# Kernel optimization log

Measured on AMD Instinct MI355X. Metric: run time of the kernel, lower is better.

The kernel has to match this reference:

```python
import jax, jax.numpy as jnp
import numpy as np

B, N_BOX, NUM_CLASSES = 32, 50, 20
FEATURE_SIZES = np.array([[52, 52], [26, 26], [13, 13]])
NUM_CENG = FEATURE_SIZES[:, 0] * FEATURE_SIZES[:, 1]            # [2704, 676, 169]
NUM_TOTAL = int((NUM_CENG * 3).sum())                            # 10647
ANCS_SCALE = np.array([[10, 13], [16, 30], [33, 23], [30, 61], [62, 45],
                       [59, 119], [116, 90], [156, 198], [373, 326]], dtype=np.float32) / 416.0
NEG_IOU_THRESHOLD = 0.5
NUM_NEG = 1000
EPS = 1e-7

def _build_anchor_grid():
    # rows ordered: level(52,26,13) -> cell (row-major) -> 3 anchors per cell
    out = []
    for lvl in range(3):
        f = int(FEATURE_SIZES[lvl, 0])
        ys, xs = np.meshgrid(np.arange(f), np.arange(f), indexing='ij')
        xy = (np.stack([xs, ys], -1).reshape(-1, 2).astype(np.float32)) / f  # cell corner (col/f,row/f)
        xy3 = np.repeat(xy, 3, axis=0)                                       # [f*f*3, 2]
        wh3 = np.tile(ANCS_SCALE[lvl * 3:(lvl + 1) * 3], (f * f, 1))
        out.append(np.concatenate([xy3, wh3], 1))
    return np.concatenate(out, 0)                                            # [10647, 4]

ANCS = jnp.asarray(_build_anchor_grid())
FSIZES = jnp.asarray(np.repeat(FEATURE_SIZES[:, 0].astype(np.float32), NUM_CENG * 3))  # [10647]
OFF_CENG = jnp.asarray([0.0, 2704.0, 3380.0])   # prefix sums of NUM_CENG
FW_LVL = jnp.asarray([52.0, 26.0, 13.0])


def _xywh2ltrb(xywh):
    return jnp.concatenate([xywh[..., :2] - xywh[..., 2:] * 0.5,
                            xywh[..., :2] + xywh[..., 2:] * 0.5], -1)


def _ciou(a, b):
    # a, b: broadcastable [..., 4] ltrb -> CIoU [...]
    lt = jnp.maximum(a[..., :2], b[..., :2])
    rb = jnp.minimum(a[..., 2:], b[..., 2:])
    wh = jnp.clip(rb - lt, 0.0)
    inter = wh[..., 0] * wh[..., 1]
    wa = a[..., 2] - a[..., 0]; ha = a[..., 3] - a[..., 1]
    wb = b[..., 2] - b[..., 0]; hb = b[..., 3] - b[..., 1]
    union = wa * ha + wb * hb - inter
    iou = inter / (union + EPS)
    clt = jnp.minimum(a[..., :2], b[..., :2])
    crb = jnp.maximum(a[..., 2:], b[..., 2:])
    cwh = crb - clt
    c2 = cwh[..., 0] ** 2 + cwh[..., 1] ** 2 + EPS
    ctr_a = (a[..., :2] + a[..., 2:]) * 0.5
    ctr_b = (b[..., :2] + b[..., 2:]) * 0.5
    rho2 = jnp.sum((ctr_a - ctr_b) ** 2, -1)
    v = (4.0 / (jnp.pi ** 2)) * (jnp.arctan(wa / (ha + EPS)) - jnp.arctan(wb / (hb + EPS))) ** 2
    alpha = jax.lax.stop_gradient(v / (1.0 - iou + v + EPS))
    return iou - rho2 / c2 - alpha * v


def _bce(p, t):
    p = jnp.clip(p, EPS, 1.0 - EPS)
    return -(t * jnp.log(p) + (1.0 - t) * jnp.log(1.0 - p))


def _per_image(p, boxes, labels):
    # p: [10647, 25], boxes: [N,4] ltrb, labels: [N] (1-based)
    N = boxes.shape[0]
    bxy = (boxes[:, :2] + boxes[:, 2:]) * 0.5
    bwh = boxes[:, 2:] - boxes[:, :2]
    # ---- anchor-target matching (source's loop always takes argmax anchor) ----
    p1xy = jnp.repeat(bxy, 9, axis=0)                                       # [N*9, 2]
    fpairs = jnp.repeat(jnp.asarray(FEATURE_SIZES, jnp.float32), 3, axis=0)  # [9, 2]
    p2f = jnp.tile(fpairs, (N, 1))                                          # [N*9, 2]
    colrow = jnp.floor(p1xy * p2f)                                          # (col, row) per box/anchor
    anc_xy = colrow / p2f
    anc_wh = jnp.tile(jnp.asarray(ANCS_SCALE), (N, 1))
    anc_ltrb = _xywh2ltrb(jnp.concatenate([anc_xy, anc_wh], 1))
    ids = jnp.arange(N, dtype=boxes.dtype)
    iou_m = _ciou(boxes[:, None, :] + ids[:, None, None],
                  anc_ltrb[None, :, :] + jnp.repeat(ids, 9)[None, :, None])  # [N, N*9]
    k = jnp.argmax(iou_m, axis=1) % 9                                       # best anchor id 0..8
    lvl = k // 3                                                            # (source quirk: //len(NUMS_ANC))
    cr = colrow[jnp.arange(N) * 9 + k]                                      # [N, 2]
    off_cr = cr[:, 1] * FW_LVL[lvl] + cr[:, 0]
    midx = ((OFF_CENG[lvl] + off_cr) * 3.0 + lvl.astype(jnp.float32)).astype(jnp.int32)  # [N]
    # ---- decode predictions ----
    p_box_xy = p[:, :2] / FSIZES[:, None] + ANCS[:, :2]
    p_box_wh = jnp.exp(p[:, 2:4]) * ANCS[:, 2:]
    p_ltrb = _xywh2ltrb(jnp.concatenate([p_box_xy, p_box_wh], -1))          # [10647, 4]
    # ---- positive losses ----
    pcls = p[midx, 5:]                                                      # [N, C]
    t = jax.nn.one_hot(labels - 1, NUM_CLASSES, dtype=pcls.dtype)
    l_cls = _bce(pcls, t).sum()
    pconf = p[midx, 4]
    l_conf_p = (-jnp.log(jnp.clip(pconf, EPS, 1.0 - EPS))).sum()
    ciou_pos = _ciou(boxes, p_ltrb[midx])                                   # [N]
    w = 2.0 - bwh[:, 0] * bwh[:, 1]
    l_box = (w * (1.0 - ciou_pos)).sum()
    # ---- negative conf loss (replicates filtered-coordinate indexing) ----
    iou_all = _ciou(boxes[:, None, :], p_ltrb[None, :, :])                  # [N, 10647]
    mx = iou_all.max(axis=0)
    mask = mx < NEG_IOU_THRESHOLD
    key = jnp.where(mask, mx, jnp.inf)
    order = jnp.argsort(key)                                                # masked-in first, ascending
    rank = jnp.cumsum(mask) - 1                                             # filtered coordinate per row
    neg_idx = rank[order][:NUM_NEG]                                         # == source's _max_index[:NUM_NEG]
    pneg = p[neg_idx, 4]
    l_conf_n = (-jnp.log(jnp.clip(1.0 - pneg, EPS, 1.0 - EPS))).sum()
    nf = jnp.asarray(N, p.dtype)
    return l_cls / nf, l_box / nf, l_conf_p / nf, l_conf_n


def setup_inputs() -> dict:
    key = jax.random.key(0)
    k1, k2, k3, k4 = jax.random.split(key, 4)
    p_yolo_ts = jax.random.uniform(k1, (B, NUM_TOTAL, 4 + 1 + NUM_CLASSES),
                                   dtype=jnp.float32, minval=1e-4, maxval=1.0 - 1e-4)
    cxy = jax.random.uniform(k2, (B, N_BOX, 2), minval=0.15, maxval=0.85)
    wh = jax.random.uniform(k3, (B, N_BOX, 2), minval=0.05, maxval=0.25)
    boxes = jnp.concatenate([cxy - wh * 0.5, cxy + wh * 0.5], -1).astype(jnp.float32)
    labels = jax.random.randint(k4, (B, N_BOX), 1, NUM_CLASSES + 1, dtype=jnp.int32)
    return {"p_yolo_ts": p_yolo_ts, "boxes": boxes, "labels": labels}


def reference(p_yolo_ts, boxes, labels):
    l_cls, l_box, l_cp, l_cn = jax.vmap(_per_image)(p_yolo_ts, boxes, labels)
    return l_cp.mean() + l_cn.mean() + l_box.mean() + l_cls.mean()
```

## Files before the change

### kernel.cpp

```cpp
#include <hip/hip_runtime.h>

namespace {

constexpr int BB   = 32;
constexpr int NBOX = 50;
constexpr int NCLS = 20;
constexpr int NT   = 10647;
constexpr int NNEG = 1000;
constexpr int DEC_BLOCKS = (NT + 63) / 64;
constexpr int POS_BLOCKS = (NBOX + 3) / 4;
constexpr float EPS = 1e-7f;
constexpr float PI4 = (float)(4.0 / 9.869604401089358);

__device__ __constant__ float c_aw[9] = {10.f/416.f,16.f/416.f,33.f/416.f,30.f/416.f,62.f/416.f,59.f/416.f,116.f/416.f,156.f/416.f,373.f/416.f};
__device__ __constant__ float c_ah[9] = {13.f/416.f,30.f/416.f,23.f/416.f,61.f/416.f,45.f/416.f,119.f/416.f,90.f/416.f,198.f/416.f,326.f/416.f};

__device__ __forceinline__ float fastrcp(float x) {
  return __builtin_amdgcn_rcpf(x);
}

__device__ __forceinline__ float dciou(float al, float at, float ar, float ab,
                                       float bl, float bt, float br, float bb,
                                       float atanA, float atanB) {
  float ltx = fmaxf(al, bl), lty = fmaxf(at, bt);
  float rbx = fminf(ar, br), rby = fminf(ab, bb);
  float wx = fmaxf(rbx - ltx, 0.f), wy = fmaxf(rby - lty, 0.f);
  float inter = wx * wy;
  float wa = ar - al, ha = ab - at;
  float wb = br - bl, hb = bb - bt;
  float uni = wa * ha + wb * hb - inter;
  float iou = inter / (uni + EPS);
  float cw = fmaxf(ar, br) - fminf(al, bl);
  float ch = fmaxf(ab, bb) - fminf(at, bt);
  float c2 = cw * cw + ch * ch + EPS;
  float dx = (al + ar) * 0.5f - (bl + br) * 0.5f;
  float dy = (at + ab) * 0.5f - (bt + bb) * 0.5f;
  float rho2 = dx * dx + dy * dy;
  float dat = atanA - atanB;
  float v = PI4 * (dat * dat);
  float alpha = v / (1.f - iou + v + EPS);
  return iou - rho2 / c2 - alpha * v;
}

__device__ __forceinline__ float dciou_h(float4 A, float4 E,
                                         float bl, float bt, float br, float bb,
                                         float areaB,
                                         float cxb, float cyb, float atanB) {
  float ltx = fmaxf(A.x, bl), lty = fmaxf(A.y, bt);
  float rbx = fminf(A.z, br), rby = fminf(A.w, bb);
  float wx = fmaxf(rbx - ltx, 0.f), wy = fmaxf(rby - lty, 0.f);
  float inter = wx * wy;
  float uni = E.w + areaB - inter;
  float iou = inter * fastrcp(uni + EPS);
  float cw = fmaxf(A.z, br) - fminf(A.x, bl);
  float ch = fmaxf(A.w, bb) - fminf(A.y, bt);
  float c2 = cw * cw + ch * ch + EPS;
  float dx = E.x - cxb;
  float dy = E.y - cyb;
  float rho2 = dx * dx + dy * dy;
  float dat = E.z - atanB;
  float v = PI4 * (dat * dat);
  float alpha = v * fastrcp(1.f - iou + v + EPS);
  return iou - rho2 * fastrcp(c2) - alpha * v;
}

__device__ __forceinline__ int wave_incl_scan(int x, int lane) {
  #pragma unroll
  for (int off = 1; off < 64; off <<= 1) {
    int y = __shfl_up(x, off);
    if (lane >= off) x += y;
  }
  return x;
}

__global__ __launch_bounds__(256) void k_main(const float* __restrict__ p,
                            const float* __restrict__ boxes,
                            const int* __restrict__ labels,
                            unsigned long long* __restrict__ comp,
                            float* __restrict__ pcls, float* __restrict__ pbox,
                            float* __restrict__ pcp) {
  const int b = blockIdx.y;
  const int tid = threadIdx.x;

  if (blockIdx.x < DEC_BLOCKS) {
    __shared__ float4 sA[NBOX];
    __shared__ float4 sE[NBOX];
    if (tid < NBOX) {
      const float* bp = boxes + (b * NBOX + tid) * 4;
      float l = bp[0], t = bp[1], r = bp[2], d = bp[3];
      sA[tid] = make_float4(l, t, r, d);
      float wa = r - l, ha = d - t;
      sE[tid] = make_float4((l + r) * 0.5f, (t + d) * 0.5f,
                            atanf(wa / (ha + EPS)), wa * ha);
    }
    __syncthreads();

    const int q = tid & 3;
    const int j = blockIdx.x * 64 + (tid >> 2);
    if (j >= NT) return;

    int lvl = (j < 8112) ? 0 : ((j < 10140) ? 1 : 2);
    int jb0 = (lvl == 0) ? 0 : ((lvl == 1) ? 8112 : 10140);
    int f   = (lvl == 0) ? 52 : ((lvl == 1) ? 26 : 13);
    int jj = j - jb0;
    int cell = jj / 3, a = jj % 3 + lvl * 3;
    int x = cell % f, y = cell / f;
    float ff = (float)f;
    const float* pr = p + ((size_t)b * NT + j) * 25;
    float px = pr[0] / ff + (float)x / ff;
    float py = pr[1] / ff + (float)y / ff;
    float pw = expf(pr[2]) * c_aw[a];
    float ph = expf(pr[3]) * c_ah[a];
    float bl = px - pw * 0.5f, bt = py - ph * 0.5f;
    float br = px + pw * 0.5f, bbv = py + ph * 0.5f;
    float wb = br - bl, hb = bbv - bt;
    float areab = wb * hb;
    float cxb = (bl + br) * 0.5f, cyb = (bt + bbv) * 0.5f;
    float atb = atanf(wb / (hb + EPS));

    float mx = -INFINITY;
    #pragma unroll 4
    for (int i = q; i < NBOX; i += 4) {
      float v = dciou_h(sA[i], sE[i], bl, bt, br, bbv, areab, cxb, cyb, atb);
      mx = fmaxf(mx, v);
    }
    mx = fmaxf(mx, __shfl_xor(mx, 1));
    mx = fmaxf(mx, __shfl_xor(mx, 2));

    if (q == 0) {
      float key = (mx < 0.5f) ? mx : INFINITY;
      unsigned int u = __float_as_uint(key);
      u = (u & 0x80000000u) ? ~u : (u | 0x80000000u);
      comp[(size_t)b * NT + j] = ((unsigned long long)u << 14) | (unsigned long long)j;
    }
  } else {
    const int lane = tid & 63;
    const int wave = tid >> 6;
    const int i = (blockIdx.x - DEC_BLOCKS) * 4 + wave;

    __shared__ float scx[NBOX], scy[NBOX];
    if (tid < NBOX) {
      const float* bp = boxes + (b * NBOX + tid) * 4;
      float l = bp[0], t = bp[1], r = bp[2], d = bp[3];
      scx[tid] = (l + r) * 0.5f;
      scy[tid] = (t + d) * 0.5f;
    }
    __syncthreads();
    if (i >= NBOX) return;

    const float* bi = boxes + (b * NBOX + i) * 4;
    float bl0 = bi[0], bt0 = bi[1], br0 = bi[2], bd0 = bi[3];
    float fi = (float)i;
    float al = bl0 + fi, at = bt0 + fi, ar = br0 + fi, ad = bd0 + fi;
    float wa = ar - al, ha = ad - at;
    float atanA = atanf(wa / (ha + EPS));

    float bestv = -INFINITY; int bestm = 1 << 30;
    #pragma unroll
    for (int m = lane; m < 9 * NBOX; m += 64) {
      int jb = m / 9, aa = m % 9;
      float fa = (aa < 3) ? 52.f : (aa < 6 ? 26.f : 13.f);
      float col = floorf(scx[jb] * fa);
      float row = floorf(scy[jb] * fa);
      float ax = col / fa, ay = row / fa;
      float aw = c_aw[aa], ah = c_ah[aa];
      float fj = (float)jb;
      float bl = (ax - aw * 0.5f) + fj;
      float bt = (ay - ah * 0.5f) + fj;
      float br = (ax + aw * 0.5f) + fj;
      float bd = (ay + ah * 0.5f) + fj;
      float wb = br - bl, hb = bd - bt;
      float atanB = atanf(wb / (hb + EPS));
      float v = dciou(al, at, ar, ad, bl, bt, br, bd, atanA, atanB);
      if (v > bestv) { bestv = v; bestm = m; }
    }
    #pragma unroll
    for (int off = 32; off > 0; off >>= 1) {
      float ov = __shfl_down(bestv, off);
      int om = __shfl_down(bestm, off);
      if (ov > bestv || (ov == bestv && om < bestm)) { bestv = ov; bestm = om; }
    }
    int bm = __shfl(bestm, 0);

    int k = bm % 9;
    int lvl = k / 3;
    float fk = (k < 3) ? 52.f : (k < 6 ? 26.f : 13.f);
    float col = floorf(scx[i] * fk);
    float row = floorf(scy[i] * fk);
    float offc = (lvl == 0) ? 0.f : (lvl == 1 ? 2704.f : 3380.f);
    int midx = (int)((offc + row * fk + col) * 3.0f + (float)lvl);

    const float* prm = p + ((size_t)b * NT + midx) * 25;
    int lab = labels[b * NBOX + i] - 1;

    float lc = 0.f;
    if (lane < NCLS) {
      float pc = prm[5 + lane];
      pc = fminf(fmaxf(pc, EPS), 1.f - EPS);
      float tt = (lane == lab) ? 1.f : 0.f;
      lc = -(tt * logf(pc) + (1.f - tt) * logf(1.f - pc));
    }
    #pragma unroll
    for (int off = 32; off > 0; off >>= 1) lc += __shfl_down(lc, off);

    if (lane == 0) {
      pcls[b * NBOX + i] = lc;
      float pc4 = prm[4];
      pc4 = fminf(fmaxf(pc4, EPS), 1.f - EPS);
      pcp[b * NBOX + i] = -logf(pc4);

      int lvl2 = (midx < 8112) ? 0 : ((midx < 10140) ? 1 : 2);
      int jb0 = (lvl2 == 0) ? 0 : ((lvl2 == 1) ? 8112 : 10140);
      int f2  = (lvl2 == 0) ? 52 : ((lvl2 == 1) ? 26 : 13);
      int jj2 = midx - jb0;
      int cell2 = jj2 / 3, a2 = jj2 % 3 + lvl2 * 3;
      int xx = cell2 % f2, yy = cell2 / f2;
      float ff2 = (float)f2;
      float px = prm[0] / ff2 + (float)xx / ff2;
      float py = prm[1] / ff2 + (float)yy / ff2;
      float pw = expf(prm[2]) * c_aw[a2];
      float ph = expf(prm[3]) * c_ah[a2];
      float pbl = px - pw * 0.5f, pbt = py - ph * 0.5f;
      float pbr = px + pw * 0.5f, pbd = py + ph * 0.5f;

      float wb = pbr - pbl, hb = pbd - pbt;
      float atanB = atanf(wb / (hb + EPS));
      float wa0 = br0 - bl0, ha0 = bd0 - bt0;
      float atanA0 = atanf(wa0 / (ha0 + EPS));
      float cp = dciou(bl0, bt0, br0, bd0, pbl, pbt, pbr, pbd, atanA0, atanB);
      float w = 2.f - wa0 * ha0;
      pbox[b * NBOX + i] = w * (1.f - cp);
    }
  }
}

__global__ __launch_bounds__(1024) void k_neg2(const unsigned long long* __restrict__ comp,
                                               const float* __restrict__ p,
                                               float* __restrict__ lcn) {
  int b = blockIdx.x;
  const unsigned long long* c = comp + (size_t)b * NT;
  const int tid = threadIdx.x, lane = tid & 63, wave = tid >> 6;

  __shared__ int hist[4096];
  __shared__ int s_w[16];
  __shared__ unsigned long long s_pref;
  __shared__ int s_rem;
  __shared__ int s_digit;
  __shared__ int s_rem_next;
  __shared__ int s_cnt;
  __shared__ float s_facc[16];
  __shared__ int s_tot[11][16];
  __shared__ int s_off[11][16];

  unsigned long long v[11];
  #pragma unroll
  for (int k = 0; k < 11; ++k) {
    int j = k * 1024 + tid;
    v[k] = (j < NT) ? c[j] : ~0ull;
  }

  int wincl[11];
  #pragma unroll
  for (int k = 0; k < 11; ++k) {
    unsigned long long x = v[k];
    int flag = ((x >> 14) < 0xFF800000ull) ? 1 : 0;
    int incl = wave_incl_scan(flag, lane);
    wincl[k] = incl;
    if (lane == 63) s_tot[k][wave] = incl;
  }
  __syncthreads();
  if (wave == 0) {
    int i0 = lane * 3;
    int a0 = (i0     < 176) ? s_tot[i0 / 16][i0 % 16] : 0;
    int a1 = (i0 + 1 < 176) ? s_tot[(i0 + 1) / 16][(i0 + 1) % 16] : 0;
    int a2 = (i0 + 2 < 176) ? s_tot[(i0 + 2) / 16][(i0 + 2) % 16] : 0;
    int lsum = a0 + a1 + a2;
    int linc = wave_incl_scan(lsum, lane);
    int lexc = linc - lsum;
    if (i0     < 176) s_off[i0 / 16][i0 % 16] = lexc;
    if (i0 + 1 < 176) s_off[(i0 + 1) / 16][(i0 + 1) % 16] = lexc + a0;
    if (i0 + 2 < 176) s_off[(i0 + 2) / 16][(i0 + 2) % 16] = lexc + a0 + a1;
    if (lane == 63) s_cnt = linc;
  }
  if (tid == 0) { s_pref = 0ull; s_rem = NNEG - 1; }
  __syncthreads();
  const bool spec = (s_cnt >= NNEG);

  for (int pass = 0; pass < 4; ++pass) {
    int lo = 36 - pass * 12;
    for (int h = tid; h < 4096; h += 1024) hist[h] = 0;
    __syncthreads();
    unsigned long long pref = s_pref;
    #pragma unroll
    for (int k = 0; k < 11; ++k) {
      unsigned long long x = v[k];
      bool fin = ((x >> 14) < 0xFF800000ull);
      if ((!spec || fin) && (x >> (lo + 12)) == (pref >> (lo + 12)))
        atomicAdd(&hist[(int)((x >> lo) & 4095ull)], 1);
    }
    __syncthreads();
    int base = tid * 4;
    int c0 = hist[base], c1 = hist[base + 1], c2 = hist[base + 2], c3 = hist[base + 3];
    int tsum = c0 + c1 + c2 + c3;
    int incl = wave_incl_scan(tsum, lane);
    if (lane == 63) s_w[wave] = incl;
    __syncthreads();
    if (wave == 0) {
      int wv = (lane < 16) ? s_w[lane] : 0;
      int wincl2 = wave_incl_scan(wv, lane);
      if (lane < 16) s_w[lane] = wincl2 - wv;
    }
    __syncthreads();
    int excl = incl - tsum + s_w[wave];
    int rem = s_rem;
    int p0 = excl, p1 = p0 + c0, p2 = p1 + c1, p3 = p2 + c2;
    if (rem >= p0 && rem < p0 + c0) { s_digit = base + 0; s_rem_next = rem - p0; }
    if (rem >= p1 && rem < p1 + c1) { s_digit = base + 1; s_rem_next = rem - p1; }
    if (rem >= p2 && rem < p2 + c2) { s_digit = base + 2; s_rem_next = rem - p2; }
    if (rem >= p3 && rem < p3 + c3) { s_digit = base + 3; s_rem_next = rem - p3; }
    __syncthreads();
    if (tid == 0) {
      s_pref |= ((unsigned long long)s_digit) << lo;
      s_rem = s_rem_next;
    }
    __syncthreads();
  }
  const unsigned long long T = s_pref;

  float acc = 0.f;
  const float* pb = p + (size_t)b * NT * 25;
  #pragma unroll
  for (int k = 0; k < 11; ++k) {
    unsigned long long x = v[k];
    if (x <= T) {
      int idx = s_off[k][wave] + wincl[k] - 1;
      if (idx < 0) idx += NT;
      float q = 1.f - pb[(size_t)idx * 25 + 4];
      q = fminf(fmaxf(q, EPS), 1.f - EPS);
      acc += -logf(q);
    }
  }

  #pragma unroll
  for (int off = 32; off > 0; off >>= 1) acc += __shfl_down(acc, off);
  if (lane == 0) s_facc[wave] = acc;
  __syncthreads();
  if (tid == 0) {
    float s = 0.f;
    #pragma unroll
    for (int w = 0; w < 16; ++w) s += s_facc[w];
    lcn[b] = s;
  }
}

__global__ void k_final(const float* __restrict__ pcls, const float* __restrict__ pbox,
                        const float* __restrict__ pcp, const float* __restrict__ lcn,
                        float* __restrict__ out) {
  int lane = threadIdx.x;
  float s = 0.f;
  if (lane < BB) {
    float a = 0.f, bx = 0.f, cp = 0.f;
    for (int i = 0; i < NBOX; ++i) {
      a  += pcls[lane * NBOX + i];
      bx += pbox[lane * NBOX + i];
      cp += pcp[lane * NBOX + i];
    }
    s = (a + bx + cp) / (float)NBOX + lcn[lane];
  }
  #pragma unroll
  for (int off = 32; off > 0; off >>= 1) s += __shfl_down(s, off);
  if (lane == 0) out[0] = s / (float)BB;
}

}

extern "C" void kernel_launch(void* const* d_in, const int* in_sizes, int n_in,
                              void* d_out, int out_size, void* d_ws, size_t ws_size,
                              hipStream_t stream) {
  const float* p      = (const float*)d_in[0];
  const float* boxes  = (const float*)d_in[1];
  const int*   labels = (const int*)d_in[2];
  float* out = (float*)d_out;

  char* ws = (char*)d_ws;
  size_t off = 0;
  unsigned long long* comp = (unsigned long long*)(ws + off); off += (size_t)BB * NT * sizeof(unsigned long long);
  float* pcls = (float*)(ws + off);                off += BB * NBOX * sizeof(float);
  float* pbox = (float*)(ws + off);                off += BB * NBOX * sizeof(float);
  float* pcp  = (float*)(ws + off);                off += BB * NBOX * sizeof(float);
  float* lcn  = (float*)(ws + off);                off += BB * sizeof(float);

  dim3 g1(DEC_BLOCKS + POS_BLOCKS, BB);
  k_main<<<g1, 256, 0, stream>>>(p, boxes, labels, comp, pcls, pbox, pcp);
  k_neg2<<<BB, 1024, 0, stream>>>(comp, p, lcn);
  k_final<<<1, 64, 0, stream>>>(pcls, pbox, pcp, lcn, out);
}
```

Before: 63.01 us.

## Fuse final reduction into negative-loss kernel and halve threads per anchor

```diff
diff --git a/kernel.cpp b/kernel.cpp
--- a/kernel.cpp
+++ b/kernel.cpp
@@ -7,7 +7,7 @@
 constexpr int NCLS = 20;
 constexpr int NT   = 10647;
 constexpr int NNEG = 1000;
-constexpr int DEC_BLOCKS = (NT + 63) / 64;
+constexpr int DEC_BLOCKS = (NT + 127) / 128;
 constexpr int POS_BLOCKS = (NBOX + 3) / 4;
 constexpr float EPS = 1e-7f;
 constexpr float PI4 = (float)(4.0 / 9.869604401089358);
@@ -78,9 +78,10 @@
                             const int* __restrict__ labels,
                             unsigned long long* __restrict__ comp,
                             float* __restrict__ pcls, float* __restrict__ pbox,
-                            float* __restrict__ pcp) {
+                            float* __restrict__ pcp, float* __restrict__ out) {
   const int b = blockIdx.y;
   const int tid = threadIdx.x;
+  if (blockIdx.x == 0 && b == 0 && tid == 0) out[0] = 0.f;
 
   if (blockIdx.x < DEC_BLOCKS) {
     __shared__ float4 sA[NBOX];
@@ -95,8 +96,8 @@
     }
     __syncthreads();
 
-    const int q = tid & 3;
-    const int j = blockIdx.x * 64 + (tid >> 2);
+    const int par = tid & 1;
+    const int j = blockIdx.x * 128 + (tid >> 1);
     if (j >= NT) return;
 
     int lvl = (j < 8112) ? 0 : ((j < 10140) ? 1 : 2);
@@ -119,15 +120,14 @@
     float atb = atanf(wb / (hb + EPS));
 
     float mx = -INFINITY;
-    #pragma unroll 4
-    for (int i = q; i < NBOX; i += 4) {
+    #pragma unroll 5
+    for (int i = par; i < NBOX; i += 2) {
       float v = dciou_h(sA[i], sE[i], bl, bt, br, bbv, areab, cxb, cyb, atb);
       mx = fmaxf(mx, v);
     }
     mx = fmaxf(mx, __shfl_xor(mx, 1));
-    mx = fmaxf(mx, __shfl_xor(mx, 2));
-
-    if (q == 0) {
+
+    if (par == 0) {
       float key = (mx < 0.5f) ? mx : INFINITY;
       unsigned int u = __float_as_uint(key);
       u = (u & 0x80000000u) ? ~u : (u | 0x80000000u);
@@ -236,7 +236,10 @@
 
 __global__ __launch_bounds__(1024) void k_neg2(const unsigned long long* __restrict__ comp,
                                                const float* __restrict__ p,
-                                               float* __restrict__ lcn) {
+                                               const float* __restrict__ pcls,
+                                               const float* __restrict__ pbox,
+                                               const float* __restrict__ pcp,
+                                               float* __restrict__ out) {
   int b = blockIdx.x;
   const unsigned long long* c = comp + (size_t)b * NT;
   const int tid = threadIdx.x, lane = tid & 63, wave = tid >> 6;
@@ -249,6 +252,7 @@
   __shared__ int s_rem_next;
   __shared__ int s_cnt;
   __shared__ float s_facc[16];
+  __shared__ float s_lcn;
   __shared__ int s_tot[11][16];
   __shared__ int s_off[11][16];
 
@@ -349,27 +353,19 @@
     float s = 0.f;
     #pragma unroll
     for (int w = 0; w < 16; ++w) s += s_facc[w];
-    lcn[b] = s;
-  }
-}
-
-__global__ void k_final(const float* __restrict__ pcls, const float* __restrict__ pbox,
-                        const float* __restrict__ pcp, const float* __restrict__ lcn,
-                        float* __restrict__ out) {
-  int lane = threadIdx.x;
-  float s = 0.f;
-  if (lane < BB) {
-    float a = 0.f, bx = 0.f, cp = 0.f;
-    for (int i = 0; i < NBOX; ++i) {
-      a  += pcls[lane * NBOX + i];
-      bx += pbox[lane * NBOX + i];
-      cp += pcp[lane * NBOX + i];
-    }
-    s = (a + bx + cp) / (float)NBOX + lcn[lane];
-  }
-  #pragma unroll
-  for (int off = 32; off > 0; off >>= 1) s += __shfl_down(s, off);
-  if (lane == 0) out[0] = s / (float)BB;
+    s_lcn = s;
+  }
+  __syncthreads();
+
+  if (wave == 0) {
+    float s3 = 0.f;
+    if (lane < NBOX)
+      s3 = pcls[b * NBOX + lane] + pbox[b * NBOX + lane] + pcp[b * NBOX + lane];
+    #pragma unroll
+    for (int off = 32; off > 0; off >>= 1) s3 += __shfl_down(s3, off);
+    if (lane == 0)
+      atomicAdd(out, (s3 / (float)NBOX + s_lcn) / (float)BB);
+  }
 }
 
 }
@@ -388,10 +384,8 @@
   float* pcls = (float*)(ws + off);                off += BB * NBOX * sizeof(float);
   float* pbox = (float*)(ws + off);                off += BB * NBOX * sizeof(float);
   float* pcp  = (float*)(ws + off);                off += BB * NBOX * sizeof(float);
-  float* lcn  = (float*)(ws + off);                off += BB * sizeof(float);
 
   dim3 g1(DEC_BLOCKS + POS_BLOCKS, BB);
-  k_main<<<g1, 256, 0, stream>>>(p, boxes, labels, comp, pcls, pbox, pcp);
-  k_neg2<<<BB, 1024, 0, stream>>>(comp, p, lcn);
-  k_final<<<1, 64, 0, stream>>>(pcls, pbox, pcp, lcn, out);
-}
+  k_main<<<g1, 256, 0, stream>>>(p, boxes, labels, comp, pcls, pbox, pcp, out);
+  k_neg2<<<BB, 1024, 0, stream>>>(comp, p, pcls, pbox, pcp, out);
+}
```

Result: faster. 56.92 us (-9.7%).
